# Kernel tuning notes

Measured on AMD Instinct MI355X. Metric: run time of the kernel, lower is better.

The kernel has to match this reference:

```python
import jax, jax.numpy as jnp
import numpy as np

B, LQ, D, DFF, NH, DH, NL, NP = 8, 1024, 256, 1024, 8, 32, 3, 4
_SHAPES = np.array([[100, 100], [50, 50], [25, 25]], dtype=np.int32)  # (H, W) per level
_AREAS = _SHAPES[:, 0] * _SHAPES[:, 1]
LIN = int(_AREAS.sum())  # 13125
_STARTS = np.concatenate([[0], np.cumsum(_AREAS)[:-1]]).astype(np.int32)


def setup_inputs() -> dict:
    key = jax.random.key(0)
    ks = iter(jax.random.split(key, 64))
    def rn(shape, s=1.0):
        return jax.random.normal(next(ks), shape, jnp.float32) * s
    return {
        "query_embed": rn((B, LQ, D)),
        "query_mask": jnp.zeros((B, LQ), bool),  # True = padded key
        "query_order": rn((B, LQ, D)),
        "values": rn((B, LIN, D)),
        "ref_point": jax.random.uniform(next(ks), (B, LQ, 2), jnp.float32),
        "ref_pos": rn((B, LQ, D)),
        "ref_feat": rn((B, LQ, D)),
        "shapes": jnp.asarray(_SHAPES),
        "level_start": jnp.asarray(_STARTS),
        "headwise_refpoint_idxs": jnp.zeros((B, LQ), jnp.int32),  # unused (side_head=0)
        # self-attention sub-block params (nn.MultiheadAttention packed in-proj)
        "sa_in_w": rn((D, 3 * D), 0.02), "sa_in_b": jnp.zeros((3 * D,)),
        "sa_out_w": rn((D, D), 0.02), "sa_out_b": jnp.zeros((D,)),
        "sa_ln1_g": jnp.ones((D,)), "sa_ln1_b": jnp.zeros((D,)),
        "sa_l1_w": rn((D, DFF), 0.02), "sa_l1_b": jnp.zeros((DFF,)),
        "sa_l2_w": rn((DFF, D), 0.02), "sa_l2_b": jnp.zeros((D,)),
        "sa_ln2_g": jnp.ones((D,)), "sa_ln2_b": jnp.zeros((D,)),
        # MDeformAttn params
        "da_val_w": rn((D, D), 0.02), "da_val_b": jnp.zeros((D,)),
        "da_off_w": rn((D, NH * NL * NP * 2), 0.001), "da_off_b": rn((NH * NL * NP * 2,), 0.01),
        "da_att_w": rn((D, NH * NL * NP), 0.02), "da_att_b": jnp.zeros((NH * NL * NP,)),
        "da_out_w": rn((D, D), 0.02), "da_out_b": jnp.zeros((D,)),
        # post-deform FFN block params
        "ln1_g": jnp.ones((D,)), "ln1_b": jnp.zeros((D,)),
        "ff1_w": rn((D, DFF), 0.02), "ff1_b": jnp.zeros((DFF,)),
        "ff2_w": rn((DFF, D), 0.02), "ff2_b": jnp.zeros((D,)),
        "ln2_g": jnp.ones((D,)), "ln2_b": jnp.zeros((D,)),
    }


def _ln(x, g, b):
    m = jnp.mean(x, -1, keepdims=True)
    v = jnp.mean((x - m) ** 2, -1, keepdims=True)
    return (x - m) / jnp.sqrt(v + 1e-5) * g + b


def _mha(q, k, v, key_padding_mask, in_w, in_b, out_w, out_b):
    Bv = q.shape[0]
    qp = (q @ in_w[:, :D] + in_b[:D]).reshape(Bv, -1, NH, DH)
    kp = (k @ in_w[:, D:2 * D] + in_b[D:2 * D]).reshape(Bv, -1, NH, DH)
    vp = (v @ in_w[:, 2 * D:] + in_b[2 * D:]).reshape(Bv, -1, NH, DH)
    scores = jnp.einsum('bqhd,bkhd->bhqk', qp, kp) / jnp.sqrt(jnp.float32(DH))
    scores = scores + jnp.where(key_padding_mask[:, None, None, :], -1e9, 0.0)
    a = jax.nn.softmax(scores, -1)
    o = jnp.einsum('bhqk,bkhd->bqhd', a, vp).reshape(Bv, -1, D)
    return o @ out_w + out_b


def _ms_deform(query, ref_point, values, shapes,
               val_w, val_b, off_w, off_b, att_w, att_b, out_w, out_b):
    # Multi-scale deformable attention (MDeformAttn, align_corners=False bilinear, zero pad)
    Bv, Lq = query.shape[0], query.shape[1]
    v = (values @ val_w + val_b).reshape(Bv, -1, NH, DH)
    off = (query @ off_w + off_b).reshape(Bv, Lq, NH, NL, NP, 2)
    attn = jax.nn.softmax((query @ att_w + att_b).reshape(Bv, Lq, NH, NL * NP), -1)
    attn = attn.reshape(Bv, Lq, NH, NL, NP)
    norm = jnp.stack([shapes[:, 1], shapes[:, 0]], -1).astype(jnp.float32)  # (W, H)
    loc = ref_point[:, :, None, None, None, :] + off / norm[None, None, None, :, None, :]
    acc = 0.0
    for lvl in range(NL):  # static spatial shapes per level
        Hl, Wl = int(_SHAPES[lvl, 0]), int(_SHAPES[lvl, 1])
        s = int(_STARTS[lvl])
        vl = v[:, s:s + Hl * Wl].transpose(0, 2, 1, 3)  # [B,NH,Hl*Wl,DH]
        ll = loc[:, :, :, lvl]                          # [B,Lq,NH,NP,2]
        x = ll[..., 0] * Wl - 0.5
        y = ll[..., 1] * Hl - 0.5
        x0 = jnp.floor(x); y0 = jnp.floor(y)
        wx = x - x0; wy = y - y0
        x0i = x0.astype(jnp.int32); y0i = y0.astype(jnp.int32)
        def tw(w):  # [B,Lq,NH,NP] -> [B,NH,Lq*NP,1]
            return w.transpose(0, 2, 1, 3).reshape(Bv, NH, -1, 1)
        def gather(yy, xx):
            valid = ((yy >= 0) & (yy < Hl) & (xx >= 0) & (xx < Wl))
            idx = jnp.clip(yy, 0, Hl - 1) * Wl + jnp.clip(xx, 0, Wl - 1)
            idx_t = idx.transpose(0, 2, 1, 3).reshape(Bv, NH, -1)
            g = jnp.take_along_axis(vl, idx_t[..., None], axis=2)  # [B,NH,Lq*NP,DH]
            return g * tw(valid.astype(vl.dtype))
        samp = (tw((1 - wy) * (1 - wx)) * gather(y0i, x0i)
                + tw((1 - wy) * wx) * gather(y0i, x0i + 1)
                + tw(wy * (1 - wx)) * gather(y0i + 1, x0i)
                + tw(wy * wx) * gather(y0i + 1, x0i + 1))
        aw = tw(attn[:, :, :, lvl])
        acc = acc + (samp * aw).reshape(Bv, NH, Lq, NP, DH).sum(3)
    out = acc.transpose(0, 2, 1, 3).reshape(Bv, Lq, D)
    return out @ out_w + out_b


def reference(query_embed, query_mask, query_order, values, ref_point, ref_pos, ref_feat,
              shapes, level_start, headwise_refpoint_idxs,
              sa_in_w, sa_in_b, sa_out_w, sa_out_b, sa_ln1_g, sa_ln1_b,
              sa_l1_w, sa_l1_b, sa_l2_w, sa_l2_b, sa_ln2_g, sa_ln2_b,
              da_val_w, da_val_b, da_off_w, da_off_b, da_att_w, da_att_b, da_out_w, da_out_b,
              ln1_g, ln1_b, ff1_w, ff1_b, ff2_w, ff2_b, ln2_g, ln2_b):
    # forward_self_att(tgt + ref_feat, query_order + ref_pos, query_mask); dropout = identity (eval)
    src = query_embed + ref_feat
    pos = query_order + ref_pos
    q = src + pos
    src = _ln(src + _mha(q, q, src, query_mask, sa_in_w, sa_in_b, sa_out_w, sa_out_b), sa_ln1_g, sa_ln1_b)
    src = _ln(src + (jax.nn.relu(src @ sa_l1_w + sa_l1_b) @ sa_l2_w + sa_l2_b), sa_ln2_g, sa_ln2_b)
    tgt = src
    dq = tgt + query_order + ref_pos + ref_feat
    tgt2 = _ms_deform(dq, ref_point, values, shapes,
                      da_val_w, da_val_b, da_off_w, da_off_b, da_att_w, da_att_b, da_out_w, da_out_b)
    tgt = _ln(tgt + tgt2, ln1_g, ln1_b)
    tgt = _ln(tgt + (jax.nn.relu(tgt @ ff1_w + ff1_b) @ ff2_w + ff2_b), ln2_g, ln2_b)
    return tgt
```

## Files before the change

### kernel.cpp

```cpp
#include <hip/hip_runtime.h>
#include <math.h>

#define B_   8
#define LQ_  1024
#define D_   256
#define NH_  8
#define DH_  32
#define LIN_ 13125

typedef __attribute__((ext_vector_type(4))) float f32x4;
typedef __attribute__((ext_vector_type(8))) short bf16x8;
typedef __attribute__((ext_vector_type(4))) short bf16x4;

__device__ __forceinline__ float4 f4add(float4 a, float4 b){
  return make_float4(a.x+b.x, a.y+b.y, a.z+b.z, a.w+b.w);
}
__device__ __forceinline__ float wredsum(float v){
  #pragma unroll
  for (int o=1;o<64;o<<=1) v += __shfl_xor(v,o,64);
  return v;
}
__device__ __forceinline__ unsigned short f2bf(float f){
  unsigned u = __float_as_uint(f);
  unsigned r = (u + 0x7fffu + ((u>>16)&1u)) >> 16;
  return (unsigned short)r;
}
__device__ __forceinline__ float bf2f(unsigned short u){
  return __uint_as_float(((unsigned)u)<<16);
}
__device__ __forceinline__ unsigned pk2(float a, float b){
  return (unsigned)f2bf(a) | ((unsigned)f2bf(b)<<16);
}
__device__ __forceinline__ float fexp2(float x){
#if __has_builtin(__builtin_amdgcn_exp2f)
  return __builtin_amdgcn_exp2f(x);
#else
  return exp2f(x);
#endif
}
__device__ __forceinline__ f32x4 mfma16x16(bf16x4 a, bf16x4 b, f32x4 c){
#if __has_builtin(__builtin_amdgcn_mfma_f32_16x16x16_bf16)
  return __builtin_amdgcn_mfma_f32_16x16x16_bf16(a, b, c, 0, 0, 0);
#else
  asm volatile("s_nop 1\n\tv_mfma_f32_16x16x16_bf16 %0, %1, %2, %0"
               : "+v"(c) : "v"(a), "v"(b));
  return c;
#endif
}
__device__ __forceinline__ void gload16(const void* g, void* l){
  __builtin_amdgcn_global_load_lds(
      (const __attribute__((address_space(1))) void*)g,
      (__attribute__((address_space(3))) void*)l, 16, 0, 0);
}
__device__ __forceinline__ int xcd_swz(int lin, int nwg){
  if (nwg < 64) return lin;
  const int q = nwg >> 3, r = nwg & 7;
  const int x = lin & 7, d = lin >> 3;
  return (x < r ? x*(q+1) : r*(q+1) + (x-r)*q) + d;
}

__global__ __launch_bounds__(256) void k_prep(
    const float4* __restrict__ qe, const float4* __restrict__ rf,
    const float4* __restrict__ qo, const float4* __restrict__ rp,
    const unsigned char* __restrict__ mask,
    const float* __restrict__ off_b, const float* __restrict__ att_b,
    float4* __restrict__ src, uint2* __restrict__ srcb, uint2* __restrict__ qb,
    float* __restrict__ biasf, float* __restrict__ biasoa)
{
  int i = blockIdx.x*256 + threadIdx.x;
  if (i < B_*LQ_) biasf[i] = mask[i] ? -2.0e9f : 0.f;
  if (blockIdx.x == 32) {
    for (int j = threadIdx.x; j < 384; j += 256)
      biasoa[j] = (j < 192) ? off_b[j] : (j < 288 ? att_b[j-192] : 0.f);
  }
  float4 s = f4add(qe[i], rf[i]);
  src[i] = s;
  float4 q = f4add(s, f4add(qo[i], rp[i]));
  srcb[i] = make_uint2(pk2(s.x,s.y), pk2(s.z,s.w));
  qb[i]   = make_uint2(pk2(q.x,q.y), pk2(q.z,q.w));
}

struct WEnt { const float* s; unsigned short* d; int K; int N; };
struct WPack { WEnt e[10]; };
__global__ __launch_bounds__(256) void k_wtcvt(WPack p)
{
  __shared__ float sm[32][33];
  WEnt w = p.e[blockIdx.y];
  const int tk = w.K >> 5, tn = w.N >> 5;
  const int nt = tk * tn;
  const int r = threadIdx.x >> 5, c = threadIdx.x & 31;
  for (int tile = blockIdx.x; tile < nt; tile += gridDim.x) {
    const int ti = tile / tn, tj = tile % tn;
    #pragma unroll
    for (int rr = r; rr < 32; rr += 8)
      sm[rr][c] = w.s[(size_t)(ti*32+rr)*w.N + tj*32 + c];
    __syncthreads();
    #pragma unroll
    for (int rr = r; rr < 32; rr += 8)
      w.d[(size_t)(tj*32+rr)*w.K + ti*32 + c] = f2bf(sm[c][rr]);
    __syncthreads();
  }
}

__global__ __launch_bounds__(256) void k_f2b8(
    const float4* __restrict__ in, uint4* __restrict__ out)
{
  const int i = blockIdx.x*256 + threadIdx.x;
  float4 a = in[2*i], b = in[2*i+1];
  out[i] = make_uint4(pk2(a.x,a.y), pk2(a.z,a.w), pk2(b.x,b.y), pk2(b.z,b.w));
}

template<bool BF16OUT>
__global__ __launch_bounds__(256) void k_gemm_bf(
    const unsigned short* __restrict__ A, int lda,
    const unsigned short* __restrict__ Wt,
    const float* __restrict__ bias,
    float* __restrict__ Cf, unsigned short* __restrict__ Cb, int ldc,
    int M, int N, int K, int relu)
{
  __shared__ unsigned short As[2][4096];
  __shared__ unsigned short Bs[2][4096];
  const int t = threadIdx.x;
  const int lin = xcd_swz(blockIdx.y*gridDim.x + blockIdx.x, gridDim.x*gridDim.y);
  const int bx = lin % gridDim.x, by = lin / gridDim.x;
  const int m0 = by * 128;
  const int n0 = bx * 128;
  const int w  = t >> 6, lane = t & 63;
  const int lr = lane & 15, lg = lane >> 4;
  const int wm = (w & 1) * 64, wn = (w >> 1) * 64;

  const int rowc  = t >> 2;
  const int cbs8  = (((t & 3) ^ ((t >> 2) & 3)) << 3);
  const size_t ra0 = (size_t)min(m0 + rowc,      M-1) * lda;
  const size_t ra1 = (size_t)min(m0 + rowc + 64, M-1) * lda;
  const size_t rb0 = (size_t)(n0 + rowc)      * K;
  const size_t rb1 = (size_t)(n0 + rowc + 64) * K;
  unsigned short* la0[2] = { &As[0][(w<<9)],        &As[1][(w<<9)] };
  unsigned short* la1[2] = { &As[0][2048+(w<<9)],   &As[1][2048+(w<<9)] };
  unsigned short* lb0[2] = { &Bs[0][(w<<9)],        &Bs[1][(w<<9)] };
  unsigned short* lb1[2] = { &Bs[0][2048+(w<<9)],   &Bs[1][2048+(w<<9)] };

  f32x4 acc[4][4];
  #pragma unroll
  for (int i=0;i<4;++i)
    #pragma unroll
    for (int j=0;j<4;++j) acc[i][j] = (f32x4){0.f,0.f,0.f,0.f};

  const int cswz = ((lg ^ (lr & 3)) << 3);
  const int nt = K >> 5;

  {
    gload16(A  + ra0 + cbs8, la0[0]);
    gload16(A  + ra1 + cbs8, la1[0]);
    gload16(Wt + rb0 + cbs8, lb0[0]);
    gload16(Wt + rb1 + cbs8, lb1[0]);
  }
  for (int ks = 0; ks < nt; ++ks) {
    const int cur = ks & 1;
    __syncthreads();
    if (ks + 1 < nt) {
      const int kb = (ks + 1) << 5;
      const int nb = cur ^ 1;
      gload16(A  + ra0 + kb + cbs8, la0[nb]);
      gload16(A  + ra1 + kb + cbs8, la1[nb]);
      gload16(Wt + rb0 + kb + cbs8, lb0[nb]);
      gload16(Wt + rb1 + kb + cbs8, lb1[nb]);
    }
    bf16x8 af[4], bfr[4];
    #pragma unroll
    for (int mi=0;mi<4;++mi)
      af[mi]  = *reinterpret_cast<const bf16x8*>(&As[cur][(wm+mi*16+lr)*32 + cswz]);
    #pragma unroll
    for (int ni=0;ni<4;++ni)
      bfr[ni] = *reinterpret_cast<const bf16x8*>(&Bs[cur][(wn+ni*16+lr)*32 + cswz]);
    #pragma unroll
    for (int mi=0;mi<4;++mi)
      #pragma unroll
      for (int ni=0;ni<4;++ni)
        acc[mi][ni] = __builtin_amdgcn_mfma_f32_16x16x32_bf16(af[mi], bfr[ni], acc[mi][ni], 0, 0, 0);
  }

  float bs[4];
  #pragma unroll
  for (int ni=0;ni<4;++ni) bs[ni] = bias[n0 + wn + ni*16 + lr];
  #pragma unroll
  for (int mi=0;mi<4;++mi){
    #pragma unroll
    for (int i=0;i<4;++i){
      const int row = m0 + wm + mi*16 + lg*4 + i;
      if (row >= M) continue;
      #pragma unroll
      for (int ni=0;ni<4;++ni){
        const int col = n0 + wn + ni*16 + lr;
        float v = acc[mi][ni][i] + bs[ni];
        if (relu) v = fmaxf(v, 0.f);
        if (BF16OUT) Cb[(size_t)row*ldc + col] = f2bf(v);
        else         Cf[(size_t)row*ldc + col] = v;
      }
    }
  }
}

template<int EPI>
__global__ __launch_bounds__(256) void k_gemm64(
    const unsigned short* __restrict__ A, int lda,
    const unsigned short* __restrict__ Wt,
    const float* __restrict__ bias,
    float* __restrict__ Cf, unsigned short* __restrict__ Cb, int ldc,
    int M, int N, int K, int relu)
{
  __shared__ unsigned short As[2][4096];
  __shared__ unsigned short Bs[2][4096];
  const int t = threadIdx.x;
  const int lin = xcd_swz(blockIdx.y*gridDim.x + blockIdx.x, gridDim.x*gridDim.y);
  const int bx = lin % gridDim.x, by = lin / gridDim.x;
  const int m0 = by * 64;
  const int n0 = bx * 64;
  const int w = t >> 6, lane = t & 63;
  const int lr = lane & 15, lg = lane >> 4;
  const int wm = (w & 1) * 32, wn = (w >> 1) * 32;

  const int c0 = w*64 + lane;
  const int c1 = 256 + w*64 + lane;
  const int r0c = c0 >> 3, s0c = ((c0 & 7) ^ (r0c & 7)) << 3;
  const int r1c = c1 >> 3, s1c = ((c1 & 7) ^ (r1c & 7)) << 3;
  const size_t a0 = (size_t)(m0 + r0c)*lda + s0c;
  const size_t a1 = (size_t)(m0 + r1c)*lda + s1c;
  const size_t b0 = (size_t)(n0 + r0c)*K + s0c;
  const size_t b1 = (size_t)(n0 + r1c)*K + s1c;
  const int d0 = w*512, d1 = 2048 + w*512;

  f32x4 acc[2][2];
  acc[0][0]=acc[0][1]=acc[1][0]=acc[1][1]=(f32x4){0.f,0.f,0.f,0.f};

  gload16(A + a0, &As[0][d0]);  gload16(A + a1, &As[0][d1]);
  gload16(Wt + b0, &Bs[0][d0]); gload16(Wt + b1, &Bs[0][d1]);
  const int nt = K >> 6;
  for (int ks = 0; ks < nt; ++ks) {
    const int cur = ks & 1;
    __syncthreads();
    if (ks + 1 < nt) {
      const int kb = (ks + 1) << 6;
      const int nb = cur ^ 1;
      gload16(A + kb + a0, &As[nb][d0]);  gload16(A + kb + a1, &As[nb][d1]);
      gload16(Wt + kb + b0, &Bs[nb][d0]); gload16(Wt + kb + b1, &Bs[nb][d1]);
    }
    bf16x8 af[2][2], bfr[2][2];
    #pragma unroll
    for (int mi=0;mi<2;++mi){
      const int r = wm + mi*16 + lr;
      #pragma unroll
      for (int kk=0;kk<2;++kk){
        const int ch = ((kk*4 + lg) ^ (r & 7)) << 3;
        af[mi][kk] = *reinterpret_cast<const bf16x8*>(&As[cur][r*64 + ch]);
      }
    }
    #pragma unroll
    for (int ni=0;ni<2;++ni){
      const int r = wn + ni*16 + lr;
      #pragma unroll
      for (int kk=0;kk<2;++kk){
        const int ch = ((kk*4 + lg) ^ (r & 7)) << 3;
        bfr[ni][kk] = *reinterpret_cast<const bf16x8*>(&Bs[cur][r*64 + ch]);
      }
    }
    #pragma unroll
    for (int kk=0;kk<2;++kk)
      #pragma unroll
      for (int mi=0;mi<2;++mi)
        #pragma unroll
        for (int ni=0;ni<2;++ni)
          acc[mi][ni] = __builtin_amdgcn_mfma_f32_16x16x32_bf16(af[mi][kk], bfr[ni][kk], acc[mi][ni], 0, 0, 0);
  }

  float bs[2];
  bs[0] = bias[n0 + wn + lr];
  bs[1] = bias[n0 + wn + 16 + lr];
  if (EPI == 3) {
    #pragma unroll
    for (int mi=0;mi<2;++mi){
      const int rowb = m0 + wm + mi*16 + lg*4;
      #pragma unroll
      for (int ni=0;ni<2;++ni){
        const int colb = n0 + wn + ni*16 + lr;
        const int bh = (rowb >> 10)*8 + (colb >> 5);
        const int d = colb & 31;
        ushort4 pkv;
        pkv.x = f2bf(acc[mi][ni][0] + bs[ni]);
        pkv.y = f2bf(acc[mi][ni][1] + bs[ni]);
        pkv.z = f2bf(acc[mi][ni][2] + bs[ni]);
        pkv.w = f2bf(acc[mi][ni][3] + bs[ni]);
        *reinterpret_cast<ushort4*>(Cb + (size_t)bh*32768 + (size_t)d*1024 + (rowb & 1023)) = pkv;
      }
    }
    return;
  }
  #pragma unroll
  for (int mi=0;mi<2;++mi){
    #pragma unroll
    for (int i=0;i<4;++i){
      const int row = m0 + wm + mi*16 + lg*4 + i;
      #pragma unroll
      for (int ni=0;ni<2;++ni){
        const int col = n0 + wn + ni*16 + lr;
        float v = acc[mi][ni][i] + bs[ni];
        if (relu) v = fmaxf(v, 0.f);
        if (EPI == 0) {
          Cf[(size_t)row*ldc + col] = v;
        } else if (EPI == 1) {
          Cb[(size_t)row*ldc + col] = f2bf(v);
        } else {
          const int ch = col & 255;
          const int sel = col >> 8;
          const int bh = (row >> 10)*8 + (ch >> 5);
          Cb[(size_t)sel*2097152 + (size_t)bh*32768 + (size_t)(row & 1023)*32 + (ch & 31)] = f2bf(v);
        }
      }
    }
  }
}

__global__ __launch_bounds__(256) void k_attn2(
    const unsigned short* __restrict__ Qbf,
    const unsigned short* __restrict__ Kbf,
    const unsigned short* __restrict__ Vtb,
    const float* __restrict__ biasf,
    unsigned short* __restrict__ Ob)
{
  __shared__ unsigned short Klds[2][2048];
  __shared__ unsigned short Vlds[2][2048];
  __shared__ float Blds[1024];
  const int t = threadIdx.x;
  const int wv = t >> 6, lane = t & 63;
  const int lin = xcd_swz(blockIdx.y*gridDim.x + blockIdx.x, gridDim.x*gridDim.y);
  const int bx = lin % gridDim.x, by = lin / gridDim.x;
  const int qt = bx * 4 + wv;
  const int bh = by;
  const int b = bh >> 3;
  const int q0 = qt << 4;
  const int lr = lane & 15, lg = lane >> 4;

  bf16x8 qf = *reinterpret_cast<const bf16x8*>(
      Qbf + (size_t)bh*32768 + (size_t)(q0 + lr)*32 + lg*8);

  *reinterpret_cast<float4*>(&Blds[t*4]) =
      *reinterpret_cast<const float4*>(biasf + b*1024 + t*4);

  const unsigned short* Kg = Kbf + (size_t)bh*32768;
  const unsigned short* Vg = Vtb + (size_t)bh*32768;

  const int kRow   = lane >> 2;
  const int kChunk = (lane & 3) ^ (kRow & 3);
  const size_t kSrc = (size_t)(wv*16 + kRow)*32 + (kChunk<<3);
  const int vDim   = lane >> 3;
  const int vChunk = (lane & 7) ^ vDim;
  const size_t vSrc = (size_t)(wv*8 + vDim)*1024 + (vChunk<<3);
  unsigned short* kDst[2] = { &Klds[0][wv<<9], &Klds[1][wv<<9] };
  unsigned short* vDst[2] = { &Vlds[0][wv<<9], &Vlds[1][wv<<9] };

  gload16(Kg + kSrc, kDst[0]);
  gload16(Vg + vSrc, vDst[0]);
  __syncthreads();

  f32x4 acc0 = {0.f,0.f,0.f,0.f}, acc1 = {0.f,0.f,0.f,0.f};
  float m_run = -1e30f, l_run = 0.f;
  const float Cs = 0.17677669529663687f * 1.4426950408889634f;
  const int kswz = (lg ^ (lr & 3)) << 3;

  for (int kt = 0; kt < 16; ++kt) {
    const int cur = kt & 1;
    if (kt + 1 < 16) {
      const size_t k0n = (size_t)(kt + 1) << 6;
      gload16(Kg + k0n*32 + kSrc, kDst[cur^1]);
      gload16(Vg + k0n    + vSrc, vDst[cur^1]);
    }
    f32x4 st[4];
    __builtin_amdgcn_s_setprio(1);
    #pragma unroll
    for (int j=0;j<4;++j){
      bf16x8 kf = *reinterpret_cast<const bf16x8*>(&Klds[cur][(16*j + lr)*32 + kswz]);
      f32x4 z = {0.f,0.f,0.f,0.f};
      st[j] = __builtin_amdgcn_mfma_f32_16x16x32_bf16(kf, qf, z, 0, 0, 0);
    }
    __builtin_amdgcn_s_setprio(0);
    const int k0 = kt << 6;
    float s[16];
    #pragma unroll
    for (int j=0;j<4;++j){
      float4 bv = *reinterpret_cast<const float4*>(&Blds[k0 + 16*j + lg*4]);
      s[4*j+0] = fmaf(st[j][0], Cs, bv.x);
      s[4*j+1] = fmaf(st[j][1], Cs, bv.y);
      s[4*j+2] = fmaf(st[j][2], Cs, bv.z);
      s[4*j+3] = fmaf(st[j][3], Cs, bv.w);
    }
    float mc = fmaxf(fmaxf(fmaxf(s[0],s[1]),fmaxf(s[2],s[3])),
                     fmaxf(fmaxf(s[4],s[5]),fmaxf(s[6],s[7])));
    float mc2 = fmaxf(fmaxf(fmaxf(s[8],s[9]),fmaxf(s[10],s[11])),
                      fmaxf(fmaxf(s[12],s[13]),fmaxf(s[14],s[15])));
    mc = fmaxf(mc, mc2);
    mc = fmaxf(mc, __shfl_xor(mc, 16, 64));
    mc = fmaxf(mc, __shfl_xor(mc, 32, 64));
    if (!__all(mc <= m_run + 8.f)) {
      float m_new = fmaxf(m_run, mc);
      float sc = fexp2(m_run - m_new);
      l_run *= sc;
      m_run = m_new;
      float sc0 = __shfl(sc, lg*4+0, 64);
      float sc1 = __shfl(sc, lg*4+1, 64);
      float sc2 = __shfl(sc, lg*4+2, 64);
      float sc3 = __shfl(sc, lg*4+3, 64);
      acc0[0]*=sc0; acc0[1]*=sc1; acc0[2]*=sc2; acc0[3]*=sc3;
      acc1[0]*=sc0; acc1[1]*=sc1; acc1[2]*=sc2; acc1[3]*=sc3;
    }
    float p[16];
    #pragma unroll
    for (int i=0;i<16;++i) p[i] = fexp2(s[i] - m_run);
    float ps = 0.f;
    #pragma unroll
    for (int i=0;i<16;++i) ps += p[i];
    ps += __shfl_xor(ps, 16, 64);
    ps += __shfl_xor(ps, 32, 64);
    l_run += ps;
    bf16x4 pb[4];
    #pragma unroll
    for (int j=0;j<4;++j){
      unsigned lo, hi;
      asm("v_cvt_pk_bf16_f32 %0, %1, %2" : "=v"(lo) : "v"(p[4*j+0]), "v"(p[4*j+1]));
      asm("v_cvt_pk_bf16_f32 %0, %1, %2" : "=v"(hi) : "v"(p[4*j+2]), "v"(p[4*j+3]));
      uint2 u = make_uint2(lo, hi);
      pb[j] = __builtin_bit_cast(bf16x4, u);
    }
    __builtin_amdgcn_s_setprio(1);
    #pragma unroll
    for (int j=0;j<4;++j){
      const int coff = (((2*j + (lg>>1)) ^ (lr & 7)) << 3) + ((lg & 1) << 2);
      bf16x4 v0 = *reinterpret_cast<const bf16x4*>(&Vlds[cur][lr*64 + coff]);
      bf16x4 v1 = *reinterpret_cast<const bf16x4*>(&Vlds[cur][(16+lr)*64 + coff]);
      acc0 = mfma16x16(pb[j], v0, acc0);
      acc1 = mfma16x16(pb[j], v1, acc1);
    }
    __builtin_amdgcn_s_setprio(0);
    __syncthreads();
  }
  float li[4];
  #pragma unroll
  for (int i=0;i<4;++i) li[i] = 1.f / __shfl(l_run, lg*4+i, 64);
  const int h = bh & 7;
  unsigned short* orow = Ob + (size_t)(b*1024 + q0)*256 + h*32;
  #pragma unroll
  for (int i=0;i<4;++i){
    orow[(size_t)(lg*4+i)*256 + lr]      = f2bf(acc0[i]*li[i]);
    orow[(size_t)(lg*4+i)*256 + 16 + lr] = f2bf(acc1[i]*li[i]);
  }
}

__global__ __launch_bounds__(256) void k_addln(
    const float* __restrict__ X, const float* __restrict__ Y,
    const float* __restrict__ g, const float* __restrict__ be,
    float* __restrict__ out, uint2* __restrict__ bout,
    const float4* __restrict__ qo, const float4* __restrict__ rp,
    const float4* __restrict__ rf, uint2* __restrict__ dqb)
{
  const int wave = threadIdx.x >> 6, lane = threadIdx.x & 63;
  const int row = blockIdx.x*4 + wave;
  const float4 x = reinterpret_cast<const float4*>(X + (size_t)row*256)[lane];
  const float4 y = reinterpret_cast<const float4*>(Y + (size_t)row*256)[lane];
  float4 v = f4add(x,y);
  float s = wredsum(v.x+v.y+v.z+v.w);
  const float mean = s * 0.00390625f;
  float4 d = make_float4(v.x-mean, v.y-mean, v.z-mean, v.w-mean);
  float sq = wredsum(d.x*d.x + d.y*d.y + d.z*d.z + d.w*d.w);
  const float rstd = rsqrtf(sq*0.00390625f + 1e-5f);
  const float4 gg = reinterpret_cast<const float4*>(g)[lane];
  const float4 bb = reinterpret_cast<const float4*>(be)[lane];
  float4 o = make_float4(d.x*rstd*gg.x + bb.x, d.y*rstd*gg.y + bb.y,
                         d.z*rstd*gg.z + bb.z, d.w*rstd*gg.w + bb.w);
  reinterpret_cast<float4*>(out + (size_t)row*256)[lane] = o;
  const size_t idx = (size_t)row*64 + lane;
  if (bout) bout[idx] = make_uint2(pk2(o.x,o.y), pk2(o.z,o.w));
  if (dqb) {
    float4 e = f4add(qo[idx], f4add(rp[idx], rf[idx]));
    float4 v2 = f4add(o, e);
    dqb[idx] = make_uint2(pk2(v2.x,v2.y), pk2(v2.z,v2.w));
  }
}

__global__ __launch_bounds__(256) void k_dgather2(
    const unsigned short* __restrict__ vproj,
    const float* __restrict__ IJ,
    const float* __restrict__ refp,
    unsigned short* __restrict__ outb)
{
  __shared__ int   ilds[8][12][4];
  __shared__ float wlds[8][12][4];
  const int t = threadIdx.x;
  const int bq = blockIdx.x;
  const int h = t >> 5;
  const int p = t & 31;
  if (p < 12) {
    const float* al = IJ + (size_t)bq*384 + 192 + h*12;
    float lg[12];
    float mx = -INFINITY;
    #pragma unroll
    for (int i=0;i<12;++i){ lg[i] = al[i]; mx = fmaxf(mx, lg[i]); }
    float se = 0.f;
    #pragma unroll
    for (int i=0;i<12;++i) se += __expf(lg[i]-mx);
    const float aw = __expf(lg[p]-mx) / se;
    const float rx = refp[(size_t)bq*2+0], ry = refp[(size_t)bq*2+1];
    const float ox = IJ[(size_t)bq*384 + h*24 + 2*p];
    const float oy = IJ[(size_t)bq*384 + h*24 + 2*p + 1];
    const int l = p >> 2;
    const int WW[3]={100,50,25}, SS[3]={0,10000,12500};
    const int Wi = WW[l], Hi = WW[l], s0 = SS[l];
    const float Wf = (float)Wi, Hf = (float)Hi;
    const float x = (rx + ox/Wf)*Wf - 0.5f;
    const float y = (ry + oy/Hf)*Hf - 0.5f;
    const float x0f = floorf(x), y0f = floorf(y);
    const float wx = x - x0f, wy = y - y0f;
    const int x0 = (int)x0f, y0 = (int)y0f;
    const int xs0 = min(max(x0,0),Wi-1),   xs1 = min(max(x0+1,0),Wi-1);
    const int ys0 = min(max(y0,0),Hi-1),   ys1 = min(max(y0+1,0),Hi-1);
    const bool vx0 = (x0>=0)&&(x0<Wi),     vx1 = (x0+1>=0)&&(x0+1<Wi);
    const bool vy0 = (y0>=0)&&(y0<Hi),     vy1 = (y0+1>=0)&&(y0+1<Hi);
    const int vb = (bq >> 10) * LIN_;
    ilds[h][p][0] = vb + s0 + ys0*Wi + xs0;
    ilds[h][p][1] = vb + s0 + ys0*Wi + xs1;
    ilds[h][p][2] = vb + s0 + ys1*Wi + xs0;
    ilds[h][p][3] = vb + s0 + ys1*Wi + xs1;
    wlds[h][p][0] = (vy0&&vx0)? (1.f-wy)*(1.f-wx)*aw : 0.f;
    wlds[h][p][1] = (vy0&&vx1)? (1.f-wy)*wx*aw       : 0.f;
    wlds[h][p][2] = (vy1&&vx0)? wy*(1.f-wx)*aw       : 0.f;
    wlds[h][p][3] = (vy1&&vx1)? wy*wx*aw             : 0.f;
  }
  __syncthreads();
  const int col = t;
  float acc = 0.f;
  #pragma unroll
  for (int pt=0; pt<12; ++pt){
    acc = fmaf(wlds[h][pt][0], bf2f(vproj[(size_t)ilds[h][pt][0]*256 + col]), acc);
    acc = fmaf(wlds[h][pt][1], bf2f(vproj[(size_t)ilds[h][pt][1]*256 + col]), acc);
    acc = fmaf(wlds[h][pt][2], bf2f(vproj[(size_t)ilds[h][pt][2]*256 + col]), acc);
    acc = fmaf(wlds[h][pt][3], bf2f(vproj[(size_t)ilds[h][pt][3]*256 + col]), acc);
  }
  outb[(size_t)bq*256 + col] = f2bf(acc);
}

extern "C" void kernel_launch(void* const* d_in, const int* in_sizes, int n_in,
                              void* d_out, int out_size, void* d_ws, size_t ws_size,
                              hipStream_t stream)
{
  const float* qe      = (const float*)d_in[0];
  const unsigned char* qmask = (const unsigned char*)d_in[1];
  const float* qo      = (const float*)d_in[2];
  const float* values  = (const float*)d_in[3];
  const float* refp    = (const float*)d_in[4];
  const float* rp      = (const float*)d_in[5];
  const float* rf      = (const float*)d_in[6];
  const float* sa_in_w = (const float*)d_in[10];
  const float* sa_in_b = (const float*)d_in[11];
  const float* sa_out_w= (const float*)d_in[12];
  const float* sa_out_b= (const float*)d_in[13];
  const float* sa_ln1_g= (const float*)d_in[14];
  const float* sa_ln1_b= (const float*)d_in[15];
  const float* sa_l1_w = (const float*)d_in[16];
  const float* sa_l1_b = (const float*)d_in[17];
  const float* sa_l2_w = (const float*)d_in[18];
  const float* sa_l2_b = (const float*)d_in[19];
  const float* sa_ln2_g= (const float*)d_in[20];
  const float* sa_ln2_b= (const float*)d_in[21];
  const float* da_val_w= (const float*)d_in[22];
  const float* da_val_b= (const float*)d_in[23];
  const float* da_off_w= (const float*)d_in[24];
  const float* da_off_b= (const float*)d_in[25];
  const float* da_att_w= (const float*)d_in[26];
  const float* da_att_b= (const float*)d_in[27];
  const float* da_out_w= (const float*)d_in[28];
  const float* da_out_b= (const float*)d_in[29];
  const float* ln1_g   = (const float*)d_in[30];
  const float* ln1_b   = (const float*)d_in[31];
  const float* ff1_w   = (const float*)d_in[32];
  const float* ff1_b   = (const float*)d_in[33];
  const float* ff2_w   = (const float*)d_in[34];
  const float* ff2_b   = (const float*)d_in[35];
  const float* ln2_g   = (const float*)d_in[36];
  const float* ln2_b   = (const float*)d_in[37];

  float* Wk = (float*)d_ws;
  const size_t MEG = 1u<<20;
  float* A   = Wk;
  float* F   = Wk + 2*MEG;
  unsigned short* Ab   = (unsigned short*)(Wk + 4*MEG);
  unsigned short* hidb = (unsigned short*)(Wk + 5*MEG);
  unsigned short* WT   = (unsigned short*)(Wk + 9*MEG);
  unsigned short* qb   = (unsigned short*)(Wk + 10*MEG);
  unsigned short* srcb = (unsigned short*)(Wk + 11*MEG);
  unsigned short* Qbf  = (unsigned short*)(Wk + 12*MEG);
  unsigned short* Kbf  = (unsigned short*)(Wk + 13*MEG);
  unsigned short* Vtb  = (unsigned short*)(Wk + 15*MEG);
  unsigned short* aob  = (unsigned short*)(Wk + 16*MEG);
  unsigned short* dqb  = (unsigned short*)(Wk + 10*MEG);
  float* IJ = Wk + 12*MEG;
  unsigned short* vb = (unsigned short*)(Wk + 23*MEG);
  unsigned short* Hb = (unsigned short*)(Wk + 37*MEG);
  unsigned short* dG = (unsigned short*)(Wk + 51*MEG);
  float* biasf  = Wk + 52*MEG;
  float* biasoa = Wk + 52*MEG + 8192;

  unsigned short* sa_inT  = WT;
  unsigned short* sa_outT = WT + 196608;
  unsigned short* sa_l1T  = WT + 262144;
  unsigned short* sa_l2T  = WT + 524288;
  unsigned short* da_valT = WT + 786432;
  unsigned short* da_outT = WT + 851968;
  unsigned short* ff1T    = WT + 917504;
  unsigned short* ff2T    = WT + 1179648;
  unsigned short* offattT = WT + 1441792;

  WPack wp_;
  wp_.e[0] = { sa_in_w, sa_inT, 256, 768 };
  wp_.e[1] = { sa_out_w, sa_outT, 256, 256 };
  wp_.e[2] = { sa_l1_w, sa_l1T, 256, 1024 };
  wp_.e[3] = { sa_l2_w, sa_l2T, 1024, 256 };
  wp_.e[4] = { da_val_w, da_valT, 256, 256 };
  wp_.e[5] = { da_out_w, da_outT, 256, 256 };
  wp_.e[6] = { ff1_w, ff1T, 256, 1024 };
  wp_.e[7] = { ff2_w, ff2T, 1024, 256 };
  wp_.e[8] = { da_off_w, offattT, 256, 192 };
  wp_.e[9] = { da_att_w, offattT + 192*256, 256, 96 };

  dim3 blk(256);
  k_wtcvt<<<dim3(64,10), blk, 0, stream>>>(wp_);
  k_f2b8<<<13125, blk, 0, stream>>>((const float4*)values, (uint4*)vb);
  k_prep<<<2048, blk, 0, stream>>>((const float4*)qe,(const float4*)rf,
                                   (const float4*)qo,(const float4*)rp,
                                   qmask, da_off_b, da_att_b,
                                   (float4*)A,(uint2*)srcb,(uint2*)qb,
                                   biasf, biasoa);
  k_gemm64<2><<<dim3(8,128), blk, 0, stream>>>(qb,256, sa_inT, sa_in_b, nullptr,Qbf,0, 8192,512,256, 0);
  k_gemm64<3><<<dim3(4,128), blk, 0, stream>>>(srcb,256, sa_inT+512*256, sa_in_b+512, nullptr,Vtb,0, 8192,256,256, 0);
  k_attn2<<<dim3(16,64), blk, 0, stream>>>(Qbf, Kbf, Vtb, biasf, aob);
  k_gemm64<0><<<dim3(4,128), blk, 0, stream>>>(aob,256, sa_outT, sa_out_b, F,nullptr,256, 8192,256,256, 0);
  k_addln<<<2048, blk, 0, stream>>>(A, F, sa_ln1_g, sa_ln1_b, A, (uint2*)Ab,
                                    nullptr, nullptr, nullptr, nullptr);
  k_gemm_bf<true><<<dim3(8,64), blk, 0, stream>>>(Ab,256, sa_l1T, sa_l1_b, nullptr,hidb,1024, 8192,1024,256, 1);
  k_gemm64<0><<<dim3(4,128), blk, 0, stream>>>(hidb,1024, sa_l2T, sa_l2_b, F,nullptr,256, 8192,256,1024, 0);
  k_addln<<<2048, blk, 0, stream>>>(A, F, sa_ln2_g, sa_ln2_b, A, (uint2*)Ab,
                                    (const float4*)qo, (const float4*)rp,
                                    (const float4*)rf, (uint2*)dqb);
  k_gemm64<0><<<dim3(6,128), blk, 0, stream>>>(dqb,256, offattT, biasoa, IJ,nullptr,384, 8192,384,256, 0);
  k_gemm_bf<true><<<dim3(2,821), blk, 0, stream>>>(vb,256, da_valT, da_val_b, nullptr,Hb,256, 105000,256,256, 0);
  k_dgather2<<<8192, blk, 0, stream>>>(Hb, IJ, refp, dG);
  k_gemm64<0><<<dim3(4,128), blk, 0, stream>>>(dG,256, da_outT, da_out_b, F,nullptr,256, 8192,256,256, 0);
  k_addln<<<2048, blk, 0, stream>>>(A, F, ln1_g, ln1_b, A, (uint2*)Ab,
                                    nullptr, nullptr, nullptr, nullptr);
  k_gemm_bf<true><<<dim3(8,64), blk, 0, stream>>>(Ab,256, ff1T, ff1_b, nullptr,hidb,1024, 8192,1024,256, 1);
  k_gemm64<0><<<dim3(4,128), blk, 0, stream>>>(hidb,1024, ff2T, ff2_b, F,nullptr,256, 8192,256,1024, 0);
  k_addln<<<2048, blk, 0, stream>>>(A, F, ln2_g, ln2_b, (float*)d_out, nullptr,
                                    nullptr, nullptr, nullptr, nullptr);
}
```

Measured before the change: 252.5 us.

## Fuse N=256 output GEMMs with residual add and LayerNorm epilogue

Replaces each 256-wide output GEMM plus separate add-LayerNorm kernel with a single kernel where each block computes a full 16-row by 256-column tile and does the residual add, LayerNorm and optional bf16/dq outputs in its epilogue. This removes the fp32 intermediate F write and reread and four kernel launches. In exchange, tiles are tall-skinny (16 rows) with large per-block B loads, giving lower weight reuse and only 512 blocks, and variance is computed in single pass E[x^2]-mean^2 form.

```diff
diff --git a/kernel.cpp b/kernel.cpp
--- a/kernel.cpp
+++ b/kernel.cpp
@@ -14,11 +14,6 @@
 
 __device__ __forceinline__ float4 f4add(float4 a, float4 b){
   return make_float4(a.x+b.x, a.y+b.y, a.z+b.z, a.w+b.w);
-}
-__device__ __forceinline__ float wredsum(float v){
-  #pragma unroll
-  for (int o=1;o<64;o<<=1) v += __shfl_xor(v,o,64);
-  return v;
 }
 __device__ __forceinline__ unsigned short f2bf(float f){
   unsigned u = __float_as_uint(f);
@@ -315,6 +310,118 @@
           const int bh = (row >> 10)*8 + (ch >> 5);
           Cb[(size_t)sel*2097152 + (size_t)bh*32768 + (size_t)(row & 1023)*32 + (ch & 31)] = f2bf(v);
         }
+      }
+    }
+  }
+}
+
+__global__ __launch_bounds__(256) void k_gemm_ln(
+    const unsigned short* __restrict__ A, int lda,
+    const unsigned short* __restrict__ Wt,
+    const float* __restrict__ bias,
+    const float* __restrict__ X,
+    const float* __restrict__ g, const float* __restrict__ be,
+    float* __restrict__ out,
+    unsigned short* __restrict__ ab,
+    const float* __restrict__ qo, const float* __restrict__ rp,
+    const float* __restrict__ rf, unsigned short* __restrict__ dqb,
+    int K)
+{
+  __shared__ unsigned short As[2][1024];
+  __shared__ unsigned short Bs[2][16384];
+  __shared__ float part[4][16][2];
+  const int t = threadIdx.x;
+  const int w = t >> 6, lane = t & 63;
+  const int lr = lane & 15, lg = lane >> 4;
+  const int m0 = xcd_swz(blockIdx.x, gridDim.x) * 16;
+
+  const int ar = t >> 3, ac = t & 7;
+  const size_t aSrc = (size_t)(m0 + ar)*lda + ((ac ^ (ar & 7)) << 3);
+  size_t bSrc[8];
+  #pragma unroll
+  for (int q=0;q<8;++q){
+    const int c = q*256 + t;
+    const int br = c >> 3, bc = c & 7;
+    bSrc[q] = (size_t)br*K + ((bc ^ (br & 7)) << 3);
+  }
+
+  f32x4 acc[4];
+  #pragma unroll
+  for (int ni=0;ni<4;++ni) acc[ni] = (f32x4){0.f,0.f,0.f,0.f};
+
+  if (w < 2) gload16(A + aSrc, &As[0][(w<<9)]);
+  #pragma unroll
+  for (int q=0;q<8;++q) gload16(Wt + bSrc[q], &Bs[0][q*2048 + (w<<9)]);
+
+  const int nt = K >> 6;
+  for (int ks = 0; ks < nt; ++ks) {
+    const int cur = ks & 1;
+    __syncthreads();
+    if (ks + 1 < nt) {
+      const int kb = (ks + 1) << 6;
+      const int nb = cur ^ 1;
+      if (w < 2) gload16(A + kb + aSrc, &As[nb][(w<<9)]);
+      #pragma unroll
+      for (int q=0;q<8;++q) gload16(Wt + kb + bSrc[q], &Bs[nb][q*2048 + (w<<9)]);
+    }
+    bf16x8 af[2];
+    #pragma unroll
+    for (int kk=0;kk<2;++kk){
+      const int ch = ((kk*4 + lg) ^ (lr & 7)) << 3;
+      af[kk] = *reinterpret_cast<const bf16x8*>(&As[cur][lr*64 + ch]);
+    }
+    #pragma unroll
+    for (int ni=0;ni<4;++ni){
+      const int r = w*64 + ni*16 + lr;
+      #pragma unroll
+      for (int kk=0;kk<2;++kk){
+        const int ch = ((kk*4 + lg) ^ (r & 7)) << 3;
+        bf16x8 bfv = *reinterpret_cast<const bf16x8*>(&Bs[cur][r*64 + ch]);
+        acc[ni] = __builtin_amdgcn_mfma_f32_16x16x32_bf16(af[kk], bfv, acc[ni], 0, 0, 0);
+      }
+    }
+  }
+
+  float v[4][4];
+  int colv[4];
+  #pragma unroll
+  for (int ni=0;ni<4;++ni) colv[ni] = w*64 + ni*16 + lr;
+  #pragma unroll
+  for (int ni=0;ni<4;++ni){
+    const float bsv = bias[colv[ni]];
+    #pragma unroll
+    for (int i=0;i<4;++i){
+      const int row = m0 + lg*4 + i;
+      v[ni][i] = acc[ni][i] + bsv + X[(size_t)row*256 + colv[ni]];
+    }
+  }
+  #pragma unroll
+  for (int i=0;i<4;++i){
+    float s1 = v[0][i]+v[1][i]+v[2][i]+v[3][i];
+    float s2 = v[0][i]*v[0][i]+v[1][i]*v[1][i]+v[2][i]*v[2][i]+v[3][i]*v[3][i];
+    #pragma unroll
+    for (int o=1;o<16;o<<=1){ s1 += __shfl_xor(s1,o,64); s2 += __shfl_xor(s2,o,64); }
+    if (lr == 0){ part[w][lg*4+i][0] = s1; part[w][lg*4+i][1] = s2; }
+  }
+  __syncthreads();
+  #pragma unroll
+  for (int i=0;i<4;++i){
+    const int rl = lg*4 + i;
+    const float S1 = part[0][rl][0]+part[1][rl][0]+part[2][rl][0]+part[3][rl][0];
+    const float S2 = part[0][rl][1]+part[1][rl][1]+part[2][rl][1]+part[3][rl][1];
+    const float mean = S1 * 0.00390625f;
+    const float var  = S2 * 0.00390625f - mean*mean;
+    const float rstd = rsqrtf(var + 1e-5f);
+    const size_t row = m0 + rl;
+    #pragma unroll
+    for (int ni=0;ni<4;++ni){
+      const int col = colv[ni];
+      const float o = (v[ni][i]-mean)*rstd*g[col] + be[col];
+      out[row*256 + col] = o;
+      if (ab) ab[row*256 + col] = f2bf(o);
+      if (dqb) {
+        const float e = qo[row*256+col] + rp[row*256+col] + rf[row*256+col];
+        dqb[row*256 + col] = f2bf(o + e);
       }
     }
   }
@@ -451,37 +558,6 @@
   for (int i=0;i<4;++i){
     orow[(size_t)(lg*4+i)*256 + lr]      = f2bf(acc0[i]*li[i]);
     orow[(size_t)(lg*4+i)*256 + 16 + lr] = f2bf(acc1[i]*li[i]);
-  }
-}
-
-__global__ __launch_bounds__(256) void k_addln(
-    const float* __restrict__ X, const float* __restrict__ Y,
-    const float* __restrict__ g, const float* __restrict__ be,
-    float* __restrict__ out, uint2* __restrict__ bout,
-    const float4* __restrict__ qo, const float4* __restrict__ rp,
-    const float4* __restrict__ rf, uint2* __restrict__ dqb)
-{
-  const int wave = threadIdx.x >> 6, lane = threadIdx.x & 63;
-  const int row = blockIdx.x*4 + wave;
-  const float4 x = reinterpret_cast<const float4*>(X + (size_t)row*256)[lane];
-  const float4 y = reinterpret_cast<const float4*>(Y + (size_t)row*256)[lane];
-  float4 v = f4add(x,y);
-  float s = wredsum(v.x+v.y+v.z+v.w);
-  const float mean = s * 0.00390625f;
-  float4 d = make_float4(v.x-mean, v.y-mean, v.z-mean, v.w-mean);
-  float sq = wredsum(d.x*d.x + d.y*d.y + d.z*d.z + d.w*d.w);
-  const float rstd = rsqrtf(sq*0.00390625f + 1e-5f);
-  const float4 gg = reinterpret_cast<const float4*>(g)[lane];
-  const float4 bb = reinterpret_cast<const float4*>(be)[lane];
-  float4 o = make_float4(d.x*rstd*gg.x + bb.x, d.y*rstd*gg.y + bb.y,
-                         d.z*rstd*gg.z + bb.z, d.w*rstd*gg.w + bb.w);
-  reinterpret_cast<float4*>(out + (size_t)row*256)[lane] = o;
-  const size_t idx = (size_t)row*64 + lane;
-  if (bout) bout[idx] = make_uint2(pk2(o.x,o.y), pk2(o.z,o.w));
-  if (dqb) {
-    float4 e = f4add(qo[idx], f4add(rp[idx], rf[idx]));
-    float4 v2 = f4add(o, e);
-    dqb[idx] = make_uint2(pk2(v2.x,v2.y), pk2(v2.z,v2.w));
   }
 }
 
@@ -589,7 +665,6 @@
   float* Wk = (float*)d_ws;
   const size_t MEG = 1u<<20;
   float* A   = Wk;
-  float* F   = Wk + 2*MEG;
   unsigned short* Ab   = (unsigned short*)(Wk + 4*MEG);
   unsigned short* hidb = (unsigned short*)(Wk + 5*MEG);
   unsigned short* WT   = (unsigned short*)(Wk + 9*MEG);
@@ -640,22 +715,21 @@
   k_gemm64<2><<<dim3(8,128), blk, 0, stream>>>(qb,256, sa_inT, sa_in_b, nullptr,Qbf,0, 8192,512,256, 0);
   k_gemm64<3><<<dim3(4,128), blk, 0, stream>>>(srcb,256, sa_inT+512*256, sa_in_b+512, nullptr,Vtb,0, 8192,256,256, 0);
   k_attn2<<<dim3(16,64), blk, 0, stream>>>(Qbf, Kbf, Vtb, biasf, aob);
-  k_gemm64<0><<<dim3(4,128), blk, 0, stream>>>(aob,256, sa_outT, sa_out_b, F,nullptr,256, 8192,256,256, 0);
-  k_addln<<<2048, blk, 0, stream>>>(A, F, sa_ln1_g, sa_ln1_b, A, (uint2*)Ab,
-                                    nullptr, nullptr, nullptr, nullptr);
+  k_gemm_ln<<<512, blk, 0, stream>>>(aob,256, sa_outT, sa_out_b, A,
+                                     sa_ln1_g, sa_ln1_b, A, Ab,
+                                     nullptr, nullptr, nullptr, nullptr, 256);
   k_gemm_bf<true><<<dim3(8,64), blk, 0, stream>>>(Ab,256, sa_l1T, sa_l1_b, nullptr,hidb,1024, 8192,1024,256, 1);
-  k_gemm64<0><<<dim3(4,128), blk, 0, stream>>>(hidb,1024, sa_l2T, sa_l2_b, F,nullptr,256, 8192,256,1024, 0);
-  k_addln<<<2048, blk, 0, stream>>>(A, F, sa_ln2_g, sa_ln2_b, A, (uint2*)Ab,
-                                    (const float4*)qo, (const float4*)rp,
-                                    (const float4*)rf, (uint2*)dqb);
+  k_gemm_ln<<<512, blk, 0, stream>>>(hidb,1024, sa_l2T, sa_l2_b, A,
+                                     sa_ln2_g, sa_ln2_b, A, Ab,
+                                     qo, rp, rf, dqb, 1024);
   k_gemm64<0><<<dim3(6,128), blk, 0, stream>>>(dqb,256, offattT, biasoa, IJ,nullptr,384, 8192,384,256, 0);
   k_gemm_bf<true><<<dim3(2,821), blk, 0, stream>>>(vb,256, da_valT, da_val_b, nullptr,Hb,256, 105000,256,256, 0);
   k_dgather2<<<8192, blk, 0, stream>>>(Hb, IJ, refp, dG);
-  k_gemm64<0><<<dim3(4,128), blk, 0, stream>>>(dG,256, da_outT, da_out_b, F,nullptr,256, 8192,256,256, 0);
-  k_addln<<<2048, blk, 0, stream>>>(A, F, ln1_g, ln1_b, A, (uint2*)Ab,
-                                    nullptr, nullptr, nullptr, nullptr);
+  k_gemm_ln<<<512, blk, 0, stream>>>(dG,256, da_outT, da_out_b, A,
+                                     ln1_g, ln1_b, A, Ab,
+                                     nullptr, nullptr, nullptr, nullptr, 256);
   k_gemm_bf<true><<<dim3(8,64), blk, 0, stream>>>(Ab,256, ff1T, ff1_b, nullptr,hidb,1024, 8192,1024,256, 1);
-  k_gemm64<0><<<dim3(4,128), blk, 0, stream>>>(hidb,1024, ff2T, ff2_b, F,nullptr,256, 8192,256,1024, 0);
-  k_addln<<<2048, blk, 0, stream>>>(A, F, ln2_g, ln2_b, (float*)d_out, nullptr,
-                                    nullptr, nullptr, nullptr, nullptr);
-}
+  k_gemm_ln<<<512, blk, 0, stream>>>(hidb,1024, ff2T, ff2_b, A,
+                                     ln2_g, ln2_b, (float*)d_out, nullptr,
+                                     nullptr, nullptr, nullptr, nullptr, 1024);
+}
```

New measurement: 243.7 us. 1.04x faster.
